# Kernel optimization log

Measured on AMD Instinct MI355X. Metric: run time of the kernel, lower is better.

The kernel has to match this reference:

```python
import jax, jax.numpy as jnp
import numpy as np

T, B, S = 32, 64, 64      # tgt_len, batch, src_len
E, H, V = 512, 1024, 32000  # embed, hidden, vocab
LE, NL = 32, 4            # lang embed size, num languages
SCALE = 0.02


def setup_inputs() -> dict:
    key = jax.random.key(0)
    ks = jax.random.split(key, 20)
    r = lambda k, shp: SCALE * jax.random.normal(k, shp, dtype=jnp.float32)
    return {
        "x": jax.random.randint(ks[0], (T, B), 0, V),
        "src_lengths": jax.random.randint(ks[1], (B,), 1, S + 1),
        "lang_idx": 0,
        "h0": jax.random.normal(ks[2], (1, B, H), dtype=jnp.float32),
        "c0": jax.random.normal(ks[3], (1, B, H), dtype=jnp.float32),
        "src_encodings": jax.random.normal(ks[4], (S, B, H), dtype=jnp.float32),
        "vocab_embed": r(ks[5], (V, E)),
        "lang_embed": r(ks[6], (NL, LE)),
        "W_wih": r(ks[7], (4 * H * E, LE)), "b_wih": r(ks[8], (4 * H * E,)),
        "W_whh": r(ks[9], (4 * H * H, LE)), "b_whh": r(ks[10], (4 * H * H,)),
        "W_bih": r(ks[11], (4 * H, LE)), "b_bih": r(ks[12], (4 * H,)),
        "W_bhh": r(ks[13], (4 * H, LE)), "b_bhh": r(ks[14], (4 * H,)),
        "c2h_W": r(ks[15], (H, 2 * H)), "c2h_b": r(ks[16], (H,)),
        "h2o_W": r(ks[17], (V, H)), "h2o_b": r(ks[18], (V,)),
    }


def reference(x, src_lengths, lang_idx, h0, c0, src_encodings,
              vocab_embed, lang_embed,
              W_wih, b_wih, W_whh, b_whh, W_bih, b_bih, W_bhh, b_bhh,
              c2h_W, c2h_b, h2o_W, h2o_b):
    hdim = c0.shape[-1]
    emb = vocab_embed[x]                       # (T,B,E)
    el = lang_embed[lang_idx]                  # (LE,)
    # hypernetwork generates the LSTM cell weights for this language
    w_ih = (W_wih @ el + b_wih).reshape(4 * hdim, -1)   # (4H,E)
    w_hh = (W_whh @ el + b_whh).reshape(4 * hdim, hdim)  # (4H,H)
    b_ih = W_bih @ el + b_bih                  # (4H,)
    b_hh = W_bhh @ el + b_bhh

    def step(carry, xt):
        h, c = carry
        gates = xt @ w_ih.T + h @ w_hh.T + b_ih + b_hh
        i, f, g, o = jnp.split(gates, 4, axis=-1)
        c = jax.nn.sigmoid(f) * c + jax.nn.sigmoid(i) * jnp.tanh(g)
        h = jax.nn.sigmoid(o) * jnp.tanh(c)
        return (h, c), h

    (hN, cN), rnn_out = jax.lax.scan(step, (h0[0], c0[0]), emb)  # rnn_out (T,B,H)

    # Luong dot attention with source-length masking
    scores = jnp.einsum('tbh,sbh->tbs', rnn_out, src_encodings)
    mask = jnp.arange(src_encodings.shape[0])[None, :] < src_lengths[:, None]  # (B,S)
    scores = jnp.where(mask[None], scores, jnp.float32(-1e30))
    attn = jax.nn.softmax(scores, axis=-1)
    context = jnp.einsum('tbs,sbh->tbh', attn, src_encodings)

    concat = jnp.concatenate([context, rnn_out], axis=-1)   # (T,B,2H)
    attn_hidden = jnp.tanh(concat @ c2h_W.T + c2h_b)         # (T,B,H)
    output = attn_hidden @ h2o_W.T + h2o_b                   # (T,B,V)
    return output, hN[None], cN[None]
```

## Files before the change

### kernel.cpp

```cpp
#include <hip/hip_runtime.h>
#include <math.h>

#define Tt 32
#define Bb 64
#define Ss 64
#define Ee 512
#define Hh 1024
#define Vv 32000
#define LEc 32
#define G4H 4096
#define Mm 2048

typedef __bf16 bf16x8 __attribute__((ext_vector_type(8)));
typedef float f32x4 __attribute__((ext_vector_type(4)));
typedef short short4v __attribute__((ext_vector_type(4)));

__device__ __forceinline__ short f2bf(float f){
  unsigned u = __builtin_bit_cast(unsigned, f);
  u += 0x7fffu + ((u >> 16) & 1u);
  return (short)(u >> 16);
}

__device__ __forceinline__ void gl_lds16(const short* g, short* l){
  __builtin_amdgcn_global_load_lds((const __attribute__((address_space(1))) void*)g,
                                   (__attribute__((address_space(3))) void*)l, 16, 0, 0);
}

__global__ __launch_bounds__(256) void k_hyper_w(
    const float* __restrict__ Wih, const float* __restrict__ bihv,
    const float* __restrict__ Whh, const float* __restrict__ bhhv,
    const float* __restrict__ lang_embed, const int* __restrict__ lang_idx,
    short* __restrict__ w_ih, short* __restrict__ w_hh)
{
  const long NIH = (long)G4H * Ee;
  const long NALL = NIH + (long)G4H * Hh;
  long r = (long)blockIdx.x * 256 + threadIdx.x;
  if (r >= NALL) return;
  const float4* el4 = (const float4*)(lang_embed + (size_t)lang_idx[0] * LEc);
  float4 e[8];
  #pragma unroll
  for (int j = 0; j < 8; j++) e[j] = el4[j];
  const float4* W4; float bb; short* outp;
  if (r < NIH){ W4 = (const float4*)(Wih + r * LEc); bb = bihv[r]; outp = w_ih + r; }
  else { long rr = r - NIH; W4 = (const float4*)(Whh + rr * LEc); bb = bhhv[rr]; outp = w_hh + rr; }
  float acc = bb;
  #pragma unroll
  for (int j = 0; j < 8; j++){
    float4 w = W4[j];
    acc += w.x*e[j].x + w.y*e[j].y + w.z*e[j].z + w.w*e[j].w;
  }
  *outp = f2bf(acc);
}

__global__ __launch_bounds__(256) void k_hyper_b(
    const float* __restrict__ Wbih, const float* __restrict__ bbih,
    const float* __restrict__ Wbhh, const float* __restrict__ bbhh,
    const float* __restrict__ lang_embed, const int* __restrict__ lang_idx,
    float* __restrict__ b_total)
{
  int u = blockIdx.x * 256 + threadIdx.x;
  if (u >= G4H) return;
  const float* el = lang_embed + (size_t)lang_idx[0] * LEc;
  float acc = bbih[u] + bbhh[u];
  #pragma unroll
  for (int j = 0; j < LEc; j++)
    acc += (Wbih[(size_t)u*LEc + j] + Wbhh[(size_t)u*LEc + j]) * el[j];
  b_total[u] = acc;
}

__global__ __launch_bounds__(256) void k_embed(
    const int* __restrict__ x, const float* __restrict__ vocab, short* __restrict__ emb)
{
  int tid = blockIdx.x * 256 + threadIdx.x;
  if (tid >= Mm * Ee / 4) return;
  int row = tid / (Ee / 4);
  int j4 = (tid % (Ee / 4)) * 4;
  int tok = x[row];
  float4 v = *(const float4*)(vocab + (size_t)tok * Ee + j4);
  short4v o = { f2bf(v.x), f2bf(v.y), f2bf(v.z), f2bf(v.w) };
  *(short4v*)(emb + (size_t)row * Ee + j4) = o;
}

__global__ __launch_bounds__(256) void k_f2bf(const float* __restrict__ in, short* __restrict__ out, long n4)
{
  long i = (long)blockIdx.x * 256 + threadIdx.x;
  if (i >= n4) return;
  float4 v = ((const float4*)in)[i];
  short4v o = { f2bf(v.x), f2bf(v.y), f2bf(v.z), f2bf(v.w) };
  ((short4v*)out)[i] = o;
}

template<int M, int N, int K, int MODE>
__global__ __launch_bounds__(256) void k_gemm(
    const short* __restrict__ A, const short* __restrict__ B,
    const float* __restrict__ bias, void* __restrict__ Cv)
{
  __shared__ short lA[4096];
  __shared__ short lB[4096];
  const int nwg = (M/128)*(N/128);
  int xcd = blockIdx.x & 7, pos = blockIdx.x >> 3;
  int wg = xcd * (nwg >> 3) + pos;
  const int MT = M/128;
  int mt = wg % MT;
  int nt = wg / MT;

  int t = threadIdx.x;
  int wave = t >> 6, lane = t & 63;
  int wm = wave >> 1, wn = wave & 1;
  int tr = t >> 2;
  int tc = (t & 3) * 8;

  const short* Agp = A + (size_t)(mt*128)*K;
  const short* Bgp = B + (size_t)(nt*128)*K;

  f32x4 acc[4][4];
  #pragma unroll
  for (int i = 0; i < 4; i++)
    #pragma unroll
    for (int j = 0; j < 4; j++) acc[i][j] = (f32x4){0.f,0.f,0.f,0.f};

  int ra = lane & 15, ko = (lane >> 4) * 8;

  for (int k0 = 0; k0 < K; k0 += 32){
    #pragma unroll
    for (int q2 = 0; q2 < 2; q2++){
      gl_lds16(Agp + (size_t)(q2*64 + tr)*K + k0 + tc, &lA[q2*2048 + wave*512]);
      gl_lds16(Bgp + (size_t)(q2*64 + tr)*K + k0 + tc, &lB[q2*2048 + wave*512]);
    }
    __syncthreads();
    bf16x8 av[4], bv[4];
    #pragma unroll
    for (int i = 0; i < 4; i++){
      av[i] = *(const bf16x8*)&lA[(wm*64 + i*16 + ra)*32 + ko];
      bv[i] = *(const bf16x8*)&lB[(wn*64 + i*16 + ra)*32 + ko];
    }
    #pragma unroll
    for (int i = 0; i < 4; i++)
      #pragma unroll
      for (int j = 0; j < 4; j++)
        acc[i][j] = __builtin_amdgcn_mfma_f32_16x16x32_bf16(av[i], bv[j], acc[i][j], 0, 0, 0);
    __syncthreads();
  }

  int col = lane & 15, r0 = (lane >> 4) * 4;
  #pragma unroll
  for (int i = 0; i < 4; i++)
    #pragma unroll
    for (int j = 0; j < 4; j++)
      #pragma unroll
      for (int q = 0; q < 4; q++){
        int m = mt*128 + wm*64 + i*16 + r0 + q;
        int n = nt*128 + wn*64 + j*16 + col;
        float v = acc[i][j][q] + bias[n];
        if (MODE == 0) ((float*)Cv)[(size_t)m * N + n] = v;
        else           ((short*)Cv)[(size_t)m * N + n] = f2bf(tanhf(v));
      }
}

#define VMW4 asm volatile("s_waitcnt vmcnt(4)" ::: "memory")
#define VMW0 asm volatile("s_waitcnt vmcnt(0)" ::: "memory")
#define VMNONE ((void)0)

#define PHASE(d, lp, LOADB, VMW, ...) do { \
    bf16x8 afr[2][2]; \
    _Pragma("unroll") \
    for (int ii = 0; ii < 2; ii++){ \
      _Pragma("unroll") \
      for (int ks = 0; ks < 2; ks++){ \
        int r = (2*(lp)+ii)*16 + la15; \
        int sc = (ks*4 + l4) ^ (r & 7); \
        afr[ii][ks] = *(const bf16x8*)(lds + ((d)*2+wm)*16384 + (r*8+sc)*16); \
      } \
    } \
    if (LOADB){ \
      _Pragma("unroll") \
      for (int fj = 0; fj < 4; fj++){ \
        _Pragma("unroll") \
        for (int ks = 0; ks < 2; ks++){ \
          int grow = wn*64 + fj*16 + la15; \
          int hh = grow >> 7, rb = grow & 127; \
          int sc = (ks*4 + l4) ^ (rb & 7); \
          bfr[fj][ks] = *(const bf16x8*)(lds + 65536 + ((d)*2+hh)*16384 + (rb*8+sc)*16); \
        } \
      } \
    } \
    __VA_ARGS__; \
    __builtin_amdgcn_s_barrier(); \
    asm volatile("s_waitcnt lgkmcnt(0)" ::: "memory"); \
    __builtin_amdgcn_sched_barrier(0); \
    __builtin_amdgcn_s_setprio(1); \
    _Pragma("unroll") \
    for (int ii = 0; ii < 2; ii++){ \
      _Pragma("unroll") \
      for (int ks = 0; ks < 2; ks++){ \
        _Pragma("unroll") \
        for (int fj = 0; fj < 4; fj++){ \
          acc[2*(lp)+ii][fj] = __builtin_amdgcn_mfma_f32_16x16x32_bf16(afr[ii][ks], bfr[fj][ks], acc[2*(lp)+ii][fj], 0, 0, 0); \
        } \
      } \
    } \
    __builtin_amdgcn_s_setprio(0); \
    VMW; \
    __builtin_amdgcn_s_barrier(); \
  } while (0)

__global__ __launch_bounds__(512, 2) void k_h2o8(
    const short* __restrict__ A, const short* __restrict__ Bw,
    const float* __restrict__ bias, float* __restrict__ C)
{
  extern __shared__ char lds[];
  int xcd = blockIdx.x & 7, pos = blockIdx.x >> 3;
  int wg = xcd * 125 + pos;
  int mt = wg % 8;
  int nt = wg / 8;

  int tid = threadIdx.x;
  int wave = tid >> 6, lane = tid & 63;
  int wm = wave >> 2, wn = wave & 3;
  int la15 = lane & 15, l4 = lane >> 4;

  const short* Ag = A  + (size_t)(mt*256)*Hh;
  const short* Bg = Bw + (size_t)(nt*256)*Hh;

  auto stage_half = [&](const short* G, int Xoff, int d, int h, int kt){
    #pragma unroll
    for (int call = 0; call < 2; call++){
      int chunk = call*512 + tid;
      int rr = chunk >> 3;
      int cc = (chunk & 7) ^ (rr & 7);
      const short* src = G + (size_t)(h*128 + rr)*Hh + kt*64 + cc*8;
      char* dst = lds + Xoff + (d*2+h)*16384 + call*8192 + wave*1024;
      gl_lds16(src, (short*)dst);
    }
  };

  f32x4 acc[8][4];
  #pragma unroll
  for (int i = 0; i < 8; i++)
    #pragma unroll
    for (int j = 0; j < 4; j++) acc[i][j] = (f32x4){0.f,0.f,0.f,0.f};
  bf16x8 bfr[4][2];

  stage_half(Ag, 0,     0, 0, 0); stage_half(Ag, 0,     0, 1, 0);
  stage_half(Bg, 65536, 0, 0, 0); stage_half(Bg, 65536, 0, 1, 0);
  stage_half(Bg, 65536, 1, 0, 1); stage_half(Bg, 65536, 1, 1, 1);
  VMW4;
  __builtin_amdgcn_s_barrier();

  for (int it = 0; it < 7; it++){
    int kt0 = 2*it;
    PHASE(0, 0, true,  VMNONE, stage_half(Ag, 0,     1, 0, kt0+1));
    PHASE(0, 1, false, VMNONE, stage_half(Ag, 0,     1, 1, kt0+1));
    PHASE(0, 2, false, VMNONE, stage_half(Bg, 65536, 0, 0, kt0+2));
    PHASE(0, 3, false, VMW4,   stage_half(Bg, 65536, 0, 1, kt0+2));
    PHASE(1, 0, true,  VMNONE, stage_half(Ag, 0,     0, 0, kt0+2));
    PHASE(1, 1, false, VMNONE, stage_half(Ag, 0,     0, 1, kt0+2));
    PHASE(1, 2, false, VMNONE, stage_half(Bg, 65536, 1, 0, kt0+3));
    PHASE(1, 3, false, VMW4,   stage_half(Bg, 65536, 1, 1, kt0+3));
  }
  PHASE(0, 0, true,  VMNONE, stage_half(Ag, 0, 1, 0, 15));
  PHASE(0, 1, false, VMNONE, stage_half(Ag, 0, 1, 1, 15));
  PHASE(0, 2, false, VMNONE, VMNONE);
  PHASE(0, 3, false, VMW0,   VMNONE);
  PHASE(1, 0, true,  VMNONE, VMNONE);
  PHASE(1, 1, false, VMNONE, VMNONE);
  PHASE(1, 2, false, VMNONE, VMNONE);
  PHASE(1, 3, false, VMNONE, VMNONE);

  int col = lane & 15, r0 = (lane >> 4) * 4;
  #pragma unroll
  for (int fi = 0; fi < 8; fi++)
    #pragma unroll
    for (int fj = 0; fj < 4; fj++)
      #pragma unroll
      for (int q = 0; q < 4; q++){
        int m = mt*256 + wm*128 + fi*16 + r0 + q;
        int n = nt*256 + wn*64 + fj*16 + col;
        C[(size_t)m * Vv + n] = acc[fi][fj][q] + bias[n];
      }
}

__global__ __launch_bounds__(256) void k_init_hc(
    const float* __restrict__ h0, const float* __restrict__ c0,
    short* __restrict__ hbf, float* __restrict__ c)
{
  int i = blockIdx.x * 256 + threadIdx.x;
  if (i >= Bb * Hh) return;
  hbf[i] = f2bf(h0[i]);
  c[i] = c0[i];
}

__global__ __launch_bounds__(256) void k_step(
    int t, const short* __restrict__ h_in, const short* __restrict__ w_hh,
    const float* __restrict__ Gx, float* __restrict__ c,
    short* __restrict__ h_out, float* __restrict__ rnn_out, short* __restrict__ concat)
{
  __shared__ float red[4][4][16][16];
  int mt = blockIdx.x >> 6;
  int n0 = (blockIdx.x & 63) * 16;
  int wv = threadIdx.x >> 6;
  int lane = threadIdx.x & 63;
  int ra = lane & 15, ko = (lane >> 4) * 8;
  f32x4 acc[4] = {{0,0,0,0},{0,0,0,0},{0,0,0,0},{0,0,0,0}};
  const short* Ap = h_in + (size_t)(mt*16 + ra) * Hh + wv*256 + ko;
  const short* Bp = w_hh + (size_t)(n0    + ra) * Hh + wv*256 + ko;
  #pragma unroll
  for (int kk = 0; kk < 256; kk += 32){
    bf16x8 a = *(const bf16x8*)(Ap + kk);
    #pragma unroll
    for (int g = 0; g < 4; g++){
      bf16x8 b = *(const bf16x8*)(Bp + (size_t)g*Hh*Hh + kk);
      acc[g] = __builtin_amdgcn_mfma_f32_16x16x32_bf16(a, b, acc[g], 0, 0, 0);
    }
  }
  int col = lane & 15, r0 = (lane >> 4) * 4;
  #pragma unroll
  for (int g = 0; g < 4; g++)
    #pragma unroll
    for (int i = 0; i < 4; i++)
      red[wv][g][r0 + i][col] = acc[g][i];
  __syncthreads();

  int r  = threadIdx.x >> 4;
  int cc = threadIdx.x & 15;
  int b  = mt*16 + r;
  int u  = n0 + cc;
  float gate[4];
  #pragma unroll
  for (int g = 0; g < 4; g++){
    float s = Gx[((size_t)t*Bb + b) * G4H + g*Hh + u];
    #pragma unroll
    for (int w2 = 0; w2 < 4; w2++) s += red[w2][g][r][cc];
    gate[g] = s;
  }
  float ig = 1.f / (1.f + expf(-gate[0]));
  float fg = 1.f / (1.f + expf(-gate[1]));
  float gg = tanhf(gate[2]);
  float og = 1.f / (1.f + expf(-gate[3]));
  size_t bu = (size_t)b * Hh + u;
  float cn = fg * c[bu] + ig * gg;
  c[bu] = cn;
  float hn = og * tanhf(cn);
  h_out[bu] = f2bf(hn);
  size_t row = (size_t)t * Bb + b;
  rnn_out[row * Hh + u] = hn;
  concat[row * (2*Hh) + Hh + u] = f2bf(hn);
}

__global__ __launch_bounds__(64) void k_scores(
    const float* __restrict__ rnn_out, const float* __restrict__ src,
    const int* __restrict__ src_len, float* __restrict__ attn)
{
  int t = blockIdx.x >> 6;
  int b = blockIdx.x & 63;
  int s = threadIdx.x;
  const float4* rp = (const float4*)(rnn_out + ((size_t)t*Bb + b) * Hh);
  const float4* sp = (const float4*)(src     + ((size_t)s*Bb + b) * Hh);
  float acc = 0.f;
  #pragma unroll 4
  for (int i = 0; i < Hh/4; i++){
    float4 rv = rp[i], sv = sp[i];
    acc += rv.x*sv.x + rv.y*sv.y + rv.z*sv.z + rv.w*sv.w;
  }
  if (s >= src_len[b]) acc = -1e30f;
  float mx = acc;
  for (int o = 32; o; o >>= 1) mx = fmaxf(mx, __shfl_xor(mx, o, 64));
  float p = expf(acc - mx);
  float sum = p;
  for (int o = 32; o; o >>= 1) sum += __shfl_xor(sum, o, 64);
  attn[((size_t)t*Bb + b) * Ss + s] = p / sum;
}

__global__ __launch_bounds__(256) void k_context(
    const float* __restrict__ attn, const float* __restrict__ src, short* __restrict__ concat)
{
  __shared__ float sat[8][64];
  int b  = blockIdx.x & 63;
  int t0 = (blockIdx.x >> 6) * 8;
  int tid = threadIdx.x;
  for (int i = tid; i < 8*64; i += 256){
    int ti = i >> 6, s = i & 63;
    sat[ti][s] = attn[((size_t)(t0 + ti)*Bb + b) * Ss + s];
  }
  __syncthreads();
  int h0 = tid * 4;
  float4 acc[8];
  #pragma unroll
  for (int i = 0; i < 8; i++) acc[i] = make_float4(0.f, 0.f, 0.f, 0.f);
  for (int s = 0; s < Ss; s++){
    float4 sv = *(const float4*)(src + ((size_t)s*Bb + b) * Hh + h0);
    #pragma unroll
    for (int i = 0; i < 8; i++){
      float a = sat[i][s];
      acc[i].x += a*sv.x; acc[i].y += a*sv.y; acc[i].z += a*sv.z; acc[i].w += a*sv.w;
    }
  }
  #pragma unroll
  for (int i = 0; i < 8; i++){
    size_t row = (size_t)(t0 + i)*Bb + b;
    short4v o = { f2bf(acc[i].x), f2bf(acc[i].y), f2bf(acc[i].z), f2bf(acc[i].w) };
    *(short4v*)(concat + row * (2*Hh) + h0) = o;
  }
}

__global__ __launch_bounds__(256) void k_final(
    const float* __restrict__ rnn_out, const float* __restrict__ c, float* __restrict__ out)
{
  int i = blockIdx.x * 256 + threadIdx.x;
  if (i >= Bb * Hh) return;
  out[(size_t)Mm * Vv + i]           = rnn_out[(size_t)(Tt-1)*Bb*Hh + i];
  out[(size_t)Mm * Vv + Bb*Hh + i]   = c[i];
}

extern "C" void kernel_launch(void* const* d_in, const int* in_sizes, int n_in,
                              void* d_out, int out_size, void* d_ws, size_t ws_size,
                              hipStream_t stream) {
  const int*   x         = (const int*)  d_in[0];
  const int*   src_len   = (const int*)  d_in[1];
  const int*   lang_idx  = (const int*)  d_in[2];
  const float* h0        = (const float*)d_in[3];
  const float* c0        = (const float*)d_in[4];
  const float* src       = (const float*)d_in[5];
  const float* vocab     = (const float*)d_in[6];
  const float* lang_emb  = (const float*)d_in[7];
  const float* Wih       = (const float*)d_in[8];
  const float* bih       = (const float*)d_in[9];
  const float* Whh       = (const float*)d_in[10];
  const float* bhh       = (const float*)d_in[11];
  const float* Wbih      = (const float*)d_in[12];
  const float* bbih      = (const float*)d_in[13];
  const float* Wbhh      = (const float*)d_in[14];
  const float* bbhh      = (const float*)d_in[15];
  const float* c2hW      = (const float*)d_in[16];
  const float* c2hb      = (const float*)d_in[17];
  const float* h2oW      = (const float*)d_in[18];
  const float* h2ob      = (const float*)d_in[19];
  float* out = (float*)d_out;

  char* ws = (char*)d_ws;
  short* w_ih   = (short*)(ws + 0);
  short* w_hh   = (short*)(ws + 4194304);
  short* c2hWb  = (short*)(ws + 12582912);
  short* h2oWb  = (short*)(ws + 16777216);
  float* b_tot  = (float*)(ws + 82313216);
  short* emb    = (short*)(ws + 82329600);
  float* Gx     = (float*)(ws + 84426752);
  short* hb0    = (short*)(ws + 117981184);
  short* hb1    = (short*)(ws + 118112256);
  float* cbuf   = (float*)(ws + 118243328);
  float* rnn    = (float*)(ws + 118505472);
  short* concat = (short*)(ws + 126894080);
  float* attn   = (float*)(ws + 135282688);
  short* ah     = (short*)(ws + 135806976);

  k_hyper_w<<<24576, 256, 0, stream>>>(Wih, bih, Whh, bhh, lang_emb, lang_idx, w_ih, w_hh);
  k_hyper_b<<<16, 256, 0, stream>>>(Wbih, bbih, Wbhh, bbhh, lang_emb, lang_idx, b_tot);
  k_embed<<<1024, 256, 0, stream>>>(x, vocab, emb);
  k_f2bf<<<2048, 256, 0, stream>>>(c2hW, c2hWb, (long)Hh*2*Hh/4);
  k_f2bf<<<32000, 256, 0, stream>>>(h2oW, h2oWb, (long)Vv*Hh/4);
  k_init_hc<<<256, 256, 0, stream>>>(h0, c0, hb0, cbuf);

  k_gemm<Mm, G4H, Ee, 0><<<(Mm/128)*(G4H/128), 256, 0, stream>>>(emb, w_ih, b_tot, Gx);

  short* hbuf[2] = { hb0, hb1 };
  for (int t = 0; t < Tt; t++){
    k_step<<<256, 256, 0, stream>>>(t, hbuf[t & 1], w_hh, Gx, cbuf,
                                    hbuf[(t + 1) & 1], rnn, concat);
  }

  k_scores<<<Tt*Bb, 64, 0, stream>>>(rnn, src, src_len, attn);
  k_context<<<256, 256, 0, stream>>>(attn, src, concat);

  k_gemm<Mm, Hh, 2*Hh, 1><<<(Mm/128)*(Hh/128), 256, 0, stream>>>(concat, c2hWb, c2hb, ah);
  hipFuncSetAttribute((const void*)k_h2o8, hipFuncAttributeMaxDynamicSharedMemorySize, 131072);
  k_h2o8<<<1000, 512, 131072, stream>>>(ah, h2oWb, h2ob, out);

  k_final<<<256, 256, 0, stream>>>(rnn, cbuf, out);
}
```

Baseline: 777.7 us.

## Overlap weight conversion with LSTM steps and fuse prep and attention kernels

Merges the hypernetwork, bias, embedding and h/c init kernels into one launch. The fp32-to-bf16 conversion of h2o and c2h weights is split into 32 slices and run by 256 extra blocks inside each recurrent step kernel, so it uses idle CUs during the latency-bound recurrence. Scores, softmax and context are fused into one kernel that tiles src/rnn through LDS, and the final h/c output copy is folded in as extra blocks. Fewer launches and hidden conversion work, but the step kernels now compete for memory bandwidth with the conversion blocks.

```diff
diff --git a/kernel.cpp b/kernel.cpp
--- a/kernel.cpp
+++ b/kernel.cpp
@@ -26,68 +26,56 @@
                                    (__attribute__((address_space(3))) void*)l, 16, 0, 0);
 }
 
-__global__ __launch_bounds__(256) void k_hyper_w(
+__global__ __launch_bounds__(256) void k_prep(
     const float* __restrict__ Wih, const float* __restrict__ bihv,
     const float* __restrict__ Whh, const float* __restrict__ bhhv,
-    const float* __restrict__ lang_embed, const int* __restrict__ lang_idx,
-    short* __restrict__ w_ih, short* __restrict__ w_hh)
-{
-  const long NIH = (long)G4H * Ee;
-  const long NALL = NIH + (long)G4H * Hh;
-  long r = (long)blockIdx.x * 256 + threadIdx.x;
-  if (r >= NALL) return;
-  const float4* el4 = (const float4*)(lang_embed + (size_t)lang_idx[0] * LEc);
-  float4 e[8];
-  #pragma unroll
-  for (int j = 0; j < 8; j++) e[j] = el4[j];
-  const float4* W4; float bb; short* outp;
-  if (r < NIH){ W4 = (const float4*)(Wih + r * LEc); bb = bihv[r]; outp = w_ih + r; }
-  else { long rr = r - NIH; W4 = (const float4*)(Whh + rr * LEc); bb = bhhv[rr]; outp = w_hh + rr; }
-  float acc = bb;
-  #pragma unroll
-  for (int j = 0; j < 8; j++){
-    float4 w = W4[j];
-    acc += w.x*e[j].x + w.y*e[j].y + w.z*e[j].z + w.w*e[j].w;
-  }
-  *outp = f2bf(acc);
-}
-
-__global__ __launch_bounds__(256) void k_hyper_b(
     const float* __restrict__ Wbih, const float* __restrict__ bbih,
     const float* __restrict__ Wbhh, const float* __restrict__ bbhh,
     const float* __restrict__ lang_embed, const int* __restrict__ lang_idx,
-    float* __restrict__ b_total)
+    const int* __restrict__ x, const float* __restrict__ vocab,
+    const float* __restrict__ h0, const float* __restrict__ c0,
+    short* __restrict__ w_ih, short* __restrict__ w_hh, float* __restrict__ b_total,
+    short* __restrict__ emb, short* __restrict__ hbf, float* __restrict__ c)
 {
-  int u = blockIdx.x * 256 + threadIdx.x;
-  if (u >= G4H) return;
-  const float* el = lang_embed + (size_t)lang_idx[0] * LEc;
-  float acc = bbih[u] + bbhh[u];
-  #pragma unroll
-  for (int j = 0; j < LEc; j++)
-    acc += (Wbih[(size_t)u*LEc + j] + Wbhh[(size_t)u*LEc + j]) * el[j];
-  b_total[u] = acc;
-}
-
-__global__ __launch_bounds__(256) void k_embed(
-    const int* __restrict__ x, const float* __restrict__ vocab, short* __restrict__ emb)
-{
-  int tid = blockIdx.x * 256 + threadIdx.x;
-  if (tid >= Mm * Ee / 4) return;
-  int row = tid / (Ee / 4);
-  int j4 = (tid % (Ee / 4)) * 4;
-  int tok = x[row];
-  float4 v = *(const float4*)(vocab + (size_t)tok * Ee + j4);
-  short4v o = { f2bf(v.x), f2bf(v.y), f2bf(v.z), f2bf(v.w) };
-  *(short4v*)(emb + (size_t)row * Ee + j4) = o;
-}
-
-__global__ __launch_bounds__(256) void k_f2bf(const float* __restrict__ in, short* __restrict__ out, long n4)
-{
-  long i = (long)blockIdx.x * 256 + threadIdx.x;
-  if (i >= n4) return;
-  float4 v = ((const float4*)in)[i];
-  short4v o = { f2bf(v.x), f2bf(v.y), f2bf(v.z), f2bf(v.w) };
-  ((short4v*)out)[i] = o;
+  int blk = blockIdx.x;
+  if (blk < 24576){
+    const long NIH = (long)G4H * Ee;
+    long r = (long)blk * 256 + threadIdx.x;
+    const float4* el4 = (const float4*)(lang_embed + (size_t)lang_idx[0] * LEc);
+    float4 e[8];
+    #pragma unroll
+    for (int j = 0; j < 8; j++) e[j] = el4[j];
+    const float4* W4; float bb; short* outp;
+    if (r < NIH){ W4 = (const float4*)(Wih + r * LEc); bb = bihv[r]; outp = w_ih + r; }
+    else { long rr = r - NIH; W4 = (const float4*)(Whh + rr * LEc); bb = bhhv[rr]; outp = w_hh + rr; }
+    float acc = bb;
+    #pragma unroll
+    for (int j = 0; j < 8; j++){
+      float4 w = W4[j];
+      acc += w.x*e[j].x + w.y*e[j].y + w.z*e[j].z + w.w*e[j].w;
+    }
+    *outp = f2bf(acc);
+  } else if (blk < 24592){
+    int u = (blk - 24576) * 256 + threadIdx.x;
+    const float* el = lang_embed + (size_t)lang_idx[0] * LEc;
+    float acc = bbih[u] + bbhh[u];
+    #pragma unroll
+    for (int j = 0; j < LEc; j++)
+      acc += (Wbih[(size_t)u*LEc + j] + Wbhh[(size_t)u*LEc + j]) * el[j];
+    b_total[u] = acc;
+  } else if (blk < 25616){
+    int tid = (blk - 24592) * 256 + threadIdx.x;
+    int row = tid / (Ee / 4);
+    int j4 = (tid % (Ee / 4)) * 4;
+    int tok = x[row];
+    float4 v = *(const float4*)(vocab + (size_t)tok * Ee + j4);
+    short4v o = { f2bf(v.x), f2bf(v.y), f2bf(v.z), f2bf(v.w) };
+    *(short4v*)(emb + (size_t)row * Ee + j4) = o;
+  } else {
+    int i = (blk - 25616) * 256 + threadIdx.x;
+    hbf[i] = f2bf(h0[i]);
+    c[i] = c0[i];
+  }
 }
 
 template<int M, int N, int K, int MODE>
@@ -280,21 +268,30 @@
       }
 }
 
-__global__ __launch_bounds__(256) void k_init_hc(
-    const float* __restrict__ h0, const float* __restrict__ c0,
-    short* __restrict__ hbf, float* __restrict__ c)
-{
-  int i = blockIdx.x * 256 + threadIdx.x;
-  if (i >= Bb * Hh) return;
-  hbf[i] = f2bf(h0[i]);
-  c[i] = c0[i];
-}
-
+#define PIG4 8716288L
+#define PIGQ 272384L
+#define H2O4 8192000L
 __global__ __launch_bounds__(256) void k_step(
     int t, const short* __restrict__ h_in, const short* __restrict__ w_hh,
     const float* __restrict__ Gx, float* __restrict__ c,
-    short* __restrict__ h_out, float* __restrict__ rnn_out, short* __restrict__ concat)
+    short* __restrict__ h_out, float* __restrict__ rnn_out, short* __restrict__ concat,
+    const float* __restrict__ h2oW, short* __restrict__ h2oWb,
+    const float* __restrict__ c2hW, short* __restrict__ c2hWb)
 {
+  if (blockIdx.x >= 256){
+    long pb = blockIdx.x - 256;
+    long base = (long)t * PIGQ;
+    for (long i = pb*256 + threadIdx.x; i < PIGQ; i += 65536){
+      long gi = base + i;
+      const float* src; short* dst;
+      if (gi < H2O4){ src = h2oW + gi*4; dst = h2oWb + gi*4; }
+      else { long j = gi - H2O4; src = c2hW + j*4; dst = c2hWb + j*4; }
+      float4 v = *(const float4*)src;
+      short4v o = { f2bf(v.x), f2bf(v.y), f2bf(v.z), f2bf(v.w) };
+      *(short4v*)dst = o;
+    }
+    return;
+  }
   __shared__ float red[4][4][16][16];
   int mt = blockIdx.x >> 6;
   int n0 = (blockIdx.x & 63) * 16;
@@ -347,42 +344,61 @@
   concat[row * (2*Hh) + Hh + u] = f2bf(hn);
 }
 
-__global__ __launch_bounds__(64) void k_scores(
+__global__ __launch_bounds__(256) void k_attn(
     const float* __restrict__ rnn_out, const float* __restrict__ src,
-    const int* __restrict__ src_len, float* __restrict__ attn)
+    const int* __restrict__ src_len, short* __restrict__ concat,
+    const float* __restrict__ cbuf, float* __restrict__ out)
 {
-  int t = blockIdx.x >> 6;
-  int b = blockIdx.x & 63;
-  int s = threadIdx.x;
-  const float4* rp = (const float4*)(rnn_out + ((size_t)t*Bb + b) * Hh);
-  const float4* sp = (const float4*)(src     + ((size_t)s*Bb + b) * Hh);
-  float acc = 0.f;
-  #pragma unroll 4
-  for (int i = 0; i < Hh/4; i++){
-    float4 rv = rp[i], sv = sp[i];
-    acc += rv.x*sv.x + rv.y*sv.y + rv.z*sv.z + rv.w*sv.w;
-  }
-  if (s >= src_len[b]) acc = -1e30f;
-  float mx = acc;
-  for (int o = 32; o; o >>= 1) mx = fmaxf(mx, __shfl_xor(mx, o, 64));
-  float p = expf(acc - mx);
-  float sum = p;
-  for (int o = 32; o; o >>= 1) sum += __shfl_xor(sum, o, 64);
-  attn[((size_t)t*Bb + b) * Ss + s] = p / sum;
-}
-
-__global__ __launch_bounds__(256) void k_context(
-    const float* __restrict__ attn, const float* __restrict__ src, short* __restrict__ concat)
-{
-  __shared__ float sat[8][64];
+  if (blockIdx.x >= 256){
+    int pb = blockIdx.x - 256;
+    for (int i = pb*256 + threadIdx.x; i < Bb*Hh; i += 1024){
+      out[(size_t)Mm * Vv + i]           = rnn_out[(size_t)(Tt-1)*Bb*Hh + i];
+      out[(size_t)Mm * Vv + Bb*Hh + i]   = cbuf[i];
+    }
+    return;
+  }
+  __shared__ float srcL[64 * 129];
+  __shared__ float rnnL[8 * 129];
+  __shared__ float satt[8][64];
+
   int b  = blockIdx.x & 63;
   int t0 = (blockIdx.x >> 6) * 8;
   int tid = threadIdx.x;
-  for (int i = tid; i < 8*64; i += 256){
-    int ti = i >> 6, s = i & 63;
-    sat[ti][s] = attn[((size_t)(t0 + ti)*Bb + b) * Ss + s];
-  }
+  int wave = tid >> 6, lane = tid & 63;
+
+  float sc0 = 0.f, sc1 = 0.f;
+  for (int c0 = 0; c0 < Hh; c0 += 128){
+    __syncthreads();
+    for (int i = tid; i < 64*128; i += 256){
+      int s = i >> 7, h = i & 127;
+      srcL[s*129 + h] = src[((size_t)s*Bb + b) * Hh + c0 + h];
+    }
+    for (int i = tid; i < 8*128; i += 256){
+      int rr = i >> 7, h = i & 127;
+      rnnL[rr*129 + h] = rnn_out[((size_t)(t0+rr)*Bb + b) * Hh + c0 + h];
+    }
+    __syncthreads();
+    const float* sp = &srcL[lane*129];
+    const float* r0p = &rnnL[(2*wave)*129];
+    const float* r1p = &rnnL[(2*wave+1)*129];
+    #pragma unroll 8
+    for (int h = 0; h < 128; h++){
+      float sv = sp[h];
+      sc0 += r0p[h] * sv;
+      sc1 += r1p[h] * sv;
+    }
+  }
+  int slen = src_len[b];
+  if (lane >= slen){ sc0 = -1e30f; sc1 = -1e30f; }
+  float mx0 = sc0, mx1 = sc1;
+  for (int o = 32; o; o >>= 1){ mx0 = fmaxf(mx0, __shfl_xor(mx0, o, 64)); mx1 = fmaxf(mx1, __shfl_xor(mx1, o, 64)); }
+  float p0 = expf(sc0 - mx0), p1 = expf(sc1 - mx1);
+  float s0 = p0, s1 = p1;
+  for (int o = 32; o; o >>= 1){ s0 += __shfl_xor(s0, o, 64); s1 += __shfl_xor(s1, o, 64); }
+  satt[2*wave][lane]   = p0 / s0;
+  satt[2*wave+1][lane] = p1 / s1;
   __syncthreads();
+
   int h0 = tid * 4;
   float4 acc[8];
   #pragma unroll
@@ -391,7 +407,7 @@
     float4 sv = *(const float4*)(src + ((size_t)s*Bb + b) * Hh + h0);
     #pragma unroll
     for (int i = 0; i < 8; i++){
-      float a = sat[i][s];
+      float a = satt[i][s];
       acc[i].x += a*sv.x; acc[i].y += a*sv.y; acc[i].z += a*sv.z; acc[i].w += a*sv.w;
     }
   }
@@ -401,15 +417,6 @@
     short4v o = { f2bf(acc[i].x), f2bf(acc[i].y), f2bf(acc[i].z), f2bf(acc[i].w) };
     *(short4v*)(concat + row * (2*Hh) + h0) = o;
   }
-}
-
-__global__ __launch_bounds__(256) void k_final(
-    const float* __restrict__ rnn_out, const float* __restrict__ c, float* __restrict__ out)
-{
-  int i = blockIdx.x * 256 + threadIdx.x;
-  if (i >= Bb * Hh) return;
-  out[(size_t)Mm * Vv + i]           = rnn_out[(size_t)(Tt-1)*Bb*Hh + i];
-  out[(size_t)Mm * Vv + Bb*Hh + i]   = c[i];
 }
 
 extern "C" void kernel_launch(void* const* d_in, const int* in_sizes, int n_in,
@@ -450,30 +457,24 @@
   float* cbuf   = (float*)(ws + 118243328);
   float* rnn    = (float*)(ws + 118505472);
   short* concat = (short*)(ws + 126894080);
-  float* attn   = (float*)(ws + 135282688);
   short* ah     = (short*)(ws + 135806976);
 
-  k_hyper_w<<<24576, 256, 0, stream>>>(Wih, bih, Whh, bhh, lang_emb, lang_idx, w_ih, w_hh);
-  k_hyper_b<<<16, 256, 0, stream>>>(Wbih, bbih, Wbhh, bbhh, lang_emb, lang_idx, b_tot);
-  k_embed<<<1024, 256, 0, stream>>>(x, vocab, emb);
-  k_f2bf<<<2048, 256, 0, stream>>>(c2hW, c2hWb, (long)Hh*2*Hh/4);
-  k_f2bf<<<32000, 256, 0, stream>>>(h2oW, h2oWb, (long)Vv*Hh/4);
-  k_init_hc<<<256, 256, 0, stream>>>(h0, c0, hb0, cbuf);
+  k_prep<<<25872, 256, 0, stream>>>(Wih, bih, Whh, bhh, Wbih, bbih, Wbhh, bbhh,
+                                    lang_emb, lang_idx, x, vocab, h0, c0,
+                                    w_ih, w_hh, b_tot, emb, hb0, cbuf);
 
   k_gemm<Mm, G4H, Ee, 0><<<(Mm/128)*(G4H/128), 256, 0, stream>>>(emb, w_ih, b_tot, Gx);
 
   short* hbuf[2] = { hb0, hb1 };
   for (int t = 0; t < Tt; t++){
-    k_step<<<256, 256, 0, stream>>>(t, hbuf[t & 1], w_hh, Gx, cbuf,
-                                    hbuf[(t + 1) & 1], rnn, concat);
-  }
-
-  k_scores<<<Tt*Bb, 64, 0, stream>>>(rnn, src, src_len, attn);
-  k_context<<<256, 256, 0, stream>>>(attn, src, concat);
+    k_step<<<512, 256, 0, stream>>>(t, hbuf[t & 1], w_hh, Gx, cbuf,
+                                    hbuf[(t + 1) & 1], rnn, concat,
+                                    h2oW, h2oWb, c2hW, c2hWb);
+  }
+
+  k_attn<<<260, 256, 0, stream>>>(rnn, src, src_len, concat, cbuf, out);
 
   k_gemm<Mm, Hh, 2*Hh, 1><<<(Mm/128)*(Hh/128), 256, 0, stream>>>(concat, c2hWb, c2hb, ah);
   hipFuncSetAttribute((const void*)k_h2o8, hipFuncAttributeMaxDynamicSharedMemorySize, 131072);
   k_h2o8<<<1000, 512, 131072, stream>>>(ah, h2oWb, h2ob, out);
-
-  k_final<<<256, 256, 0, stream>>>(rnn, cbuf, out);
-}
+}
```

Result: faster. 738.3 us (-5.1%).
